# Kernel optimization log

Hardware: AMD Instinct MI355X
Metric: run time of the kernel (lower is better)

Reference implementation:

```python
import jax, jax.numpy as jnp
import numpy as np

N = 50000
F_IN = 128
HID = 16
CLS = 40
NEG_SLOPE = 0.2


def gat_layer(x, src, dst, W, a_src, a_dst, b, heads, out_ch):
    # x: [N, Fin]; src/dst: [E] (self-loops included); W: [Fin, heads*out_ch]
    n = x.shape[0]
    h = (x @ W).reshape(n, heads, out_ch)                    # [N, H, C]
    al_s = jnp.einsum('nhc,hc->nh', h, a_src)                # [N, H]
    al_d = jnp.einsum('nhc,hc->nh', h, a_dst)                # [N, H]
    e = jax.nn.leaky_relu(al_s[src] + al_d[dst], NEG_SLOPE)  # [E, H]
    # segment softmax over incoming edges of each dst node
    m = jax.ops.segment_max(e, dst, num_segments=n)          # [N, H]
    ex = jnp.exp(e - m[dst])
    den = jax.ops.segment_sum(ex, dst, num_segments=n)
    alpha = ex / den[dst]                                    # [E, H]
    out = jax.ops.segment_sum(h[src] * alpha[:, :, None], dst, num_segments=n)
    return out.reshape(n, heads * out_ch) + b


def setup_inputs() -> dict:
    key = jax.random.key(0)
    ks = jax.random.split(key, 16)
    E = 800000
    x = jax.random.normal(ks[0], (N, F_IN), dtype=jnp.float32)
    edge_index = jax.random.randint(ks[1], (2, E), 0, N, dtype=jnp.int64)
    s = 0.1
    W1 = jax.random.normal(ks[2], (F_IN, 7 * HID), dtype=jnp.float32) * s
    a_src1 = jax.random.normal(ks[3], (7, HID), dtype=jnp.float32) * s
    a_dst1 = jax.random.normal(ks[4], (7, HID), dtype=jnp.float32) * s
    b1 = jnp.zeros((7 * HID,), dtype=jnp.float32)
    W2 = jax.random.normal(ks[5], (7 * HID, 6 * HID), dtype=jnp.float32) * s
    a_src2 = jax.random.normal(ks[6], (6, HID), dtype=jnp.float32) * s
    a_dst2 = jax.random.normal(ks[7], (6, HID), dtype=jnp.float32) * s
    b2 = jnp.zeros((6 * HID,), dtype=jnp.float32)
    W3 = jax.random.normal(ks[8], (6 * HID, 6 * CLS), dtype=jnp.float32) * s
    a_src3 = jax.random.normal(ks[9], (6, CLS), dtype=jnp.float32) * s
    a_dst3 = jax.random.normal(ks[10], (6, CLS), dtype=jnp.float32) * s
    b3 = jnp.zeros((6 * CLS,), dtype=jnp.float32)
    return {
        'x': x, 'edge_index': edge_index,
        'W1': W1, 'a_src1': a_src1, 'a_dst1': a_dst1, 'b1': b1,
        'W2': W2, 'a_src2': a_src2, 'a_dst2': a_dst2, 'b2': b2,
        'W3': W3, 'a_src3': a_src3, 'a_dst3': a_dst3, 'b3': b3,
    }


def reference(x, edge_index, W1, a_src1, a_dst1, b1, W2, a_src2, a_dst2, b2, W3, a_src3, a_dst3, b3):
    # add self-loops once (PyG GATConv default add_self_loops=True)
    loops = jnp.arange(N, dtype=edge_index.dtype)
    src = jnp.concatenate([edge_index[0], loops])
    dst = jnp.concatenate([edge_index[1], loops])
    # dropout layers are identity in eval mode
    h = gat_layer(x, src, dst, W1, a_src1, a_dst1, b1, 7, HID)
    h = jax.nn.relu(h)
    h = gat_layer(h, src, dst, W2, a_src2, a_dst2, b2, 6, HID)
    h = jax.nn.relu(h)
    out = gat_layer(h, src, dst, W3, a_src3, a_dst3, b3, 6, CLS)
    return out
```

## Files before the change

kernel.cpp:

```cpp
#include <hip/hip_runtime.h>
#include <hip/hip_fp16.h>
#include <cstdint>

#define NNODES 50000

__device__ inline void wave_lds_fence() {
  asm volatile("s_waitcnt lgkmcnt(0)" ::: "memory");
  __builtin_amdgcn_wave_barrier();
}

__global__ void hist_kernel(const int* __restrict__ ei, int E, int Nn, int* __restrict__ cnt) {
  int i = blockIdx.x * blockDim.x + threadIdx.x;
  int ET = E + Nn;
  if (i >= ET) return;
  int d = (i < E) ? ei[E + i] : (i - E);
  atomicAdd(&cnt[d], 1);
}

__global__ void scan1_kernel(const int* __restrict__ in, int n, int* __restrict__ incl,
                             int* __restrict__ bsum) {
  __shared__ int sd[256];
  int g = blockIdx.x * 256 + threadIdx.x;
  int v = (g < n) ? in[g] : 0;
  sd[threadIdx.x] = v;
  __syncthreads();
  for (int off = 1; off < 256; off <<= 1) {
    int t = (threadIdx.x >= off) ? sd[threadIdx.x - off] : 0;
    __syncthreads();
    sd[threadIdx.x] += t;
    __syncthreads();
  }
  if (g < n) incl[g] = sd[threadIdx.x];
  if (threadIdx.x == 255) bsum[blockIdx.x] = sd[255];
}

__global__ void scan3_kernel(const int* __restrict__ incl, const int* __restrict__ bscan,
                             int n, int* __restrict__ rowptr) {
  int g = blockIdx.x * 256 + threadIdx.x;
  if (g == 0) rowptr[0] = 0;
  if (g < n) {
    int off = (blockIdx.x > 0) ? bscan[blockIdx.x - 1] : 0;
    rowptr[g + 1] = incl[g] + off;
  }
}

__global__ void scatter_kernel(const int* __restrict__ ei, int E, int Nn,
                               const int* __restrict__ rowptr, int* __restrict__ cnt2,
                               int* __restrict__ esorted) {
  int i = blockIdx.x * blockDim.x + threadIdx.x;
  int ET = E + Nn;
  if (i >= ET) return;
  int s, d;
  if (i < E) { s = ei[i]; d = ei[E + i]; }
  else       { s = i - E; d = i - E; }
  int pos = rowptr[d] + atomicAdd(&cnt2[d], 1);
  esorted[pos] = s;
}

template <int FIN, int H, int C, int HCP, int BLOCK>
__global__ __launch_bounds__(BLOCK) void gemm_alpha_kernel(const float* __restrict__ X,
                                                           const float* __restrict__ W,
                                                           const float* __restrict__ a_s,
                                                           const float* __restrict__ a_d,
                                                           __half* __restrict__ Hout,
                                                           float* __restrict__ als8,
                                                           float* __restrict__ ald8) {
  constexpr int HC = H * C;
  constexpr int NT = 16;
  constexpr int TM = 4, TN = 4;
  constexpr int CG = HC / TN;
  constexpr int MAXC = C / TN;
  constexpr int PF = 8;
  static_assert(FIN % (2 * PF) == 0, "FIN must be a multiple of 16");
  __shared__ __align__(16) float xs[FIN * NT];
  __shared__ float redS[NT][H][MAXC];
  __shared__ float redD[NT][H][MAXC];
  const int n0 = blockIdx.x * NT;
  for (int i = threadIdx.x * 4; i < NT * FIN; i += BLOCK * 4) {
    float4 v = *(const float4*)(X + (size_t)n0 * FIN + i);
    int node = i / FIN, k = i % FIN;
    xs[(k + 0) * NT + node] = v.x;
    xs[(k + 1) * NT + node] = v.y;
    xs[(k + 2) * NT + node] = v.z;
    xs[(k + 3) * NT + node] = v.w;
  }
  __syncthreads();
  const int cg = threadIdx.x % CG;
  const int ng = threadIdx.x / CG;
  const bool compute = (ng < NT / TM);
  const int c0 = cg * TN;
  const int i0 = ng * TM;
  if (compute) {
    float acc[TM][TN];
#pragma unroll
    for (int i = 0; i < TM; ++i)
#pragma unroll
      for (int j = 0; j < TN; ++j) acc[i][j] = 0.f;
    const float* Wp = W + c0;
    float4 wb[PF], wn[PF];
#pragma unroll
    for (int j = 0; j < PF; ++j) wb[j] = *(const float4*)(Wp + (size_t)j * HC);
#pragma unroll 1
    for (int k0 = 0; k0 < FIN; k0 += 2 * PF) {
#pragma unroll
      for (int j = 0; j < PF; ++j) wn[j] = *(const float4*)(Wp + (size_t)(k0 + PF + j) * HC);
#pragma unroll
      for (int j = 0; j < PF; ++j) {
        const float4 xv = *(const float4*)(xs + (k0 + j) * NT + i0);
        const float4 wv = wb[j];
        acc[0][0] += xv.x * wv.x; acc[0][1] += xv.x * wv.y; acc[0][2] += xv.x * wv.z; acc[0][3] += xv.x * wv.w;
        acc[1][0] += xv.y * wv.x; acc[1][1] += xv.y * wv.y; acc[1][2] += xv.y * wv.z; acc[1][3] += xv.y * wv.w;
        acc[2][0] += xv.z * wv.x; acc[2][1] += xv.z * wv.y; acc[2][2] += xv.z * wv.z; acc[2][3] += xv.z * wv.w;
        acc[3][0] += xv.w * wv.x; acc[3][1] += xv.w * wv.y; acc[3][2] += xv.w * wv.z; acc[3][3] += xv.w * wv.w;
      }
      const int kp = (k0 + 2 * PF < FIN) ? (k0 + 2 * PF) : 0;
#pragma unroll
      for (int j = 0; j < PF; ++j) wb[j] = *(const float4*)(Wp + (size_t)(kp + j) * HC);
#pragma unroll
      for (int j = 0; j < PF; ++j) {
        const float4 xv = *(const float4*)(xs + (k0 + PF + j) * NT + i0);
        const float4 wv = wn[j];
        acc[0][0] += xv.x * wv.x; acc[0][1] += xv.x * wv.y; acc[0][2] += xv.x * wv.z; acc[0][3] += xv.x * wv.w;
        acc[1][0] += xv.y * wv.x; acc[1][1] += xv.y * wv.y; acc[1][2] += xv.y * wv.z; acc[1][3] += xv.y * wv.w;
        acc[2][0] += xv.z * wv.x; acc[2][1] += xv.z * wv.y; acc[2][2] += xv.z * wv.z; acc[2][3] += xv.z * wv.w;
        acc[3][0] += xv.w * wv.x; acc[3][1] += xv.w * wv.y; acc[3][2] += xv.w * wv.z; acc[3][3] += xv.w * wv.w;
      }
    }
#pragma unroll
    for (int i = 0; i < TM; ++i) {
      union { __half2 h2[2]; uint2 u; } pk;
      pk.h2[0] = __floats2half2_rn(acc[i][0], acc[i][1]);
      pk.h2[1] = __floats2half2_rn(acc[i][2], acc[i][3]);
      *(uint2*)(Hout + (size_t)(n0 + i0 + i) * HCP + c0) = pk.u;
    }
    const int hd = c0 / C;
    const int cidx = (c0 % C) / TN;
    const float4 as4 = *(const float4*)(a_s + c0);
    const float4 ad4 = *(const float4*)(a_d + c0);
#pragma unroll
    for (int i = 0; i < TM; ++i) {
      float ps = acc[i][0] * as4.x + acc[i][1] * as4.y + acc[i][2] * as4.z + acc[i][3] * as4.w;
      float pd = acc[i][0] * ad4.x + acc[i][1] * ad4.y + acc[i][2] * ad4.z + acc[i][3] * ad4.w;
      redS[i0 + i][hd][cidx] = ps;
      redD[i0 + i][hd][cidx] = pd;
    }
  }
  __syncthreads();
  for (int z = threadIdx.x; z < NT * H; z += BLOCK) {
    int n = z / H, h = z % H;
    float ss = 0.f, dd = 0.f;
#pragma unroll
    for (int c = 0; c < MAXC; ++c) { ss += redS[n][h][c]; dd += redD[n][h][c]; }
    als8[(size_t)(n0 + n) * 8 + h] = ss;
    ald8[(size_t)(n0 + n) * 8 + h] = dd;
  }
}

template <int H, int C, int HCP, int RELU>
__global__ __launch_bounds__(256) void agg_kernel(const __half* __restrict__ Hbuf,
                                                  const float* __restrict__ als8,
                                                  const float* __restrict__ ald8,
                                                  const int* __restrict__ rowptr,
                                                  const int* __restrict__ esrc,
                                                  const float* __restrict__ bias,
                                                  float* __restrict__ Out, int n_nodes) {
  constexpr int HC = H * C;
  constexpr int NCHUNK = HC / 8;
  constexpr int GROUPS = (NCHUNK <= 16) ? 4 : 2;
  constexpr int LPG = 64 / GROUPS;
  constexpr int UN = 3;
  constexpr int TPAD = 72;
  const int wave = threadIdx.x >> 6;
  const int lane = threadIdx.x & 63;
  const int grp = lane / LPG;
  const int lg = lane % LPG;
  const int n = blockIdx.x * 4 + wave;
  __shared__ float s_w[4][TPAD * H];
  __shared__ int s_src[4][TPAD];
  if (n >= n_nodes) return;

  if (lane < TPAD - 64) s_src[wave][64 + lane] = 0;
  for (int z = lane; z < (TPAD - 64) * H; z += 64) s_w[wave][64 * H + z] = 0.f;

  const int e0 = rowptr[n];
  const int e1 = rowptr[n + 1];

  float aldn[H];
#pragma unroll
  for (int h = 0; h < H; ++h) aldn[h] = ald8[n * 8 + h];

  const int head = min((lg * 8) / C, H - 1);
  const bool act = lg < NCHUNK;

  float acc[8];
  float lsum = 0.f;
#pragma unroll
  for (int j = 0; j < 8; ++j) acc[j] = 0.f;

  for (int base = e0; base < e1; base += 64) {
    const int cnt = (e1 - base < 64) ? (e1 - base) : 64;
    int sreg = 0;
    if (lane < cnt) sreg = esrc[base + lane];
    s_src[wave][lane] = sreg;
    if (lane < cnt) {
      const float4 qa = *(const float4*)(als8 + (size_t)sreg * 8);
      const float4 qb = *(const float4*)(als8 + (size_t)sreg * 8 + 4);
      const float q[8] = {qa.x, qa.y, qa.z, qa.w, qb.x, qb.y, qb.z, qb.w};
#pragma unroll
      for (int h = 0; h < H; ++h) {
        float v = q[h] + aldn[h];
        v = v > 0.f ? v : 0.2f * v;
        s_w[wave][lane * H + h] = __expf(v);
      }
    } else {
#pragma unroll
      for (int h = 0; h < H; ++h) s_w[wave][lane * H + h] = 0.f;
    }
    wave_lds_fence();
    const int nit = (cnt + GROUPS - 1) / GROUPS;
    for (int i = 0; i < nit; i += UN) {
      int tt[UN], si[UN];
      uint4 v[UN];
      float w[UN];
#pragma unroll
      for (int k = 0; k < UN; ++k) tt[k] = (i + k) * GROUPS + grp;
#pragma unroll
      for (int k = 0; k < UN; ++k) si[k] = s_src[wave][tt[k]];
#pragma unroll
      for (int k = 0; k < UN; ++k)
        if (act) v[k] = *(const uint4*)(Hbuf + (size_t)si[k] * HCP + lg * 8);
#pragma unroll
      for (int k = 0; k < UN; ++k) w[k] = s_w[wave][tt[k] * H + head];
#pragma unroll
      for (int k = 0; k < UN; ++k)
        if (act) {
          const __half2* hp = (const __half2*)&v[k];
          float2 f0 = __half22float2(hp[0]);
          float2 f1 = __half22float2(hp[1]);
          float2 f2 = __half22float2(hp[2]);
          float2 f3 = __half22float2(hp[3]);
          lsum += w[k];
          acc[0] += w[k] * f0.x; acc[1] += w[k] * f0.y;
          acc[2] += w[k] * f1.x; acc[3] += w[k] * f1.y;
          acc[4] += w[k] * f2.x; acc[5] += w[k] * f2.y;
          acc[6] += w[k] * f3.x; acc[7] += w[k] * f3.y;
        }
    }
    wave_lds_fence();
  }

#pragma unroll
  for (int off = LPG; off < 64; off <<= 1) {
    lsum += __shfl_xor(lsum, off);
#pragma unroll
    for (int j = 0; j < 8; ++j) acc[j] += __shfl_xor(acc[j], off);
  }

  if (grp == 0 && act) {
    const float inv = 1.f / lsum;
    const float4 b0 = *(const float4*)(bias + lg * 8);
    const float4 b1 = *(const float4*)(bias + lg * 8 + 4);
    float4 o0, o1;
    o0.x = acc[0] * inv + b0.x; o0.y = acc[1] * inv + b0.y;
    o0.z = acc[2] * inv + b0.z; o0.w = acc[3] * inv + b0.w;
    o1.x = acc[4] * inv + b1.x; o1.y = acc[5] * inv + b1.y;
    o1.z = acc[6] * inv + b1.z; o1.w = acc[7] * inv + b1.w;
    if (RELU) {
      o0.x = fmaxf(o0.x, 0.f); o0.y = fmaxf(o0.y, 0.f);
      o0.z = fmaxf(o0.z, 0.f); o0.w = fmaxf(o0.w, 0.f);
      o1.x = fmaxf(o1.x, 0.f); o1.y = fmaxf(o1.y, 0.f);
      o1.z = fmaxf(o1.z, 0.f); o1.w = fmaxf(o1.w, 0.f);
    }
    *(float4*)(Out + (size_t)n * HC + lg * 8) = o0;
    *(float4*)(Out + (size_t)n * HC + lg * 8 + 4) = o1;
  }
}

extern "C" void kernel_launch(void* const* d_in, const int* in_sizes, int n_in,
                              void* d_out, int out_size, void* d_ws, size_t ws_size,
                              hipStream_t stream) {
  const int N = NNODES;
  const float* x  = (const float*)d_in[0];
  const int* ei   = (const int*)d_in[1];
  const float* W1 = (const float*)d_in[2];
  const float* as1 = (const float*)d_in[3];
  const float* ad1 = (const float*)d_in[4];
  const float* b1  = (const float*)d_in[5];
  const float* W2  = (const float*)d_in[6];
  const float* as2 = (const float*)d_in[7];
  const float* ad2 = (const float*)d_in[8];
  const float* b2  = (const float*)d_in[9];
  const float* W3  = (const float*)d_in[10];
  const float* as3 = (const float*)d_in[11];
  const float* ad3 = (const float*)d_in[12];
  const float* b3  = (const float*)d_in[13];
  float* out = (float*)d_out;
  const int E = in_sizes[1] / 2;
  const int ET = E + N;

  char* ws = (char*)d_ws;
  size_t off = 0;
  auto alloc = [&](size_t bytes) -> char* {
    char* p = ws + off;
    off += (bytes + 255) & ~(size_t)255;
    return p;
  };
  int* cnt     = (int*)alloc((size_t)N * 4);
  int* cnt2    = (int*)alloc((size_t)N * 4);
  int* incl    = (int*)alloc((size_t)N * 4);
  int* bsum    = (int*)alloc(512 * 4);
  int* bscan   = (int*)alloc(256 * 4);
  int* rowptr  = (int*)alloc((size_t)(N + 1) * 4);
  int* esorted = (int*)alloc((size_t)ET * 4);
  float* als   = (float*)alloc((size_t)N * 8 * 4);
  float* ald   = (float*)alloc((size_t)N * 8 * 4);
  __half* hbuf = (__half*)alloc((size_t)N * 256 * 2);
  float* abuf  = (float*)alloc((size_t)N * 112 * 4);

  hipMemsetAsync(cnt, 0, (size_t)N * 4, stream);
  hipMemsetAsync(cnt2, 0, (size_t)N * 4, stream);

  const int B1 = (N + 255) / 256;
  hist_kernel<<<(ET + 255) / 256, 256, 0, stream>>>(ei, E, N, cnt);
  scan1_kernel<<<B1, 256, 0, stream>>>(cnt, N, incl, bsum);
  scan1_kernel<<<1, 256, 0, stream>>>(bsum, B1, bscan, bsum + 256);
  scan3_kernel<<<B1, 256, 0, stream>>>(incl, bscan, N, rowptr);
  scatter_kernel<<<(ET + 255) / 256, 256, 0, stream>>>(ei, E, N, rowptr, cnt2, esorted);

  gemm_alpha_kernel<128, 7, 16, 128, 128><<<N / 16, 128, 0, stream>>>(x, W1, as1, ad1, hbuf, als, ald);
  agg_kernel<7, 16, 128, 1><<<(N + 3) / 4, 256, 0, stream>>>(hbuf, als, ald, rowptr, esorted, b1, abuf, N);
  gemm_alpha_kernel<112, 6, 16, 96, 128><<<N / 16, 128, 0, stream>>>(abuf, W2, as2, ad2, hbuf, als, ald);
  agg_kernel<6, 16, 96, 1><<<(N + 3) / 4, 256, 0, stream>>>(hbuf, als, ald, rowptr, esorted, b2, abuf, N);
  gemm_alpha_kernel<96, 6, 40, 256, 256><<<N / 16, 256, 0, stream>>>(abuf, W3, as3, ad3, hbuf, als, ald);
  agg_kernel<6, 40, 256, 0><<<(N + 3) / 4, 256, 0, stream>>>(hbuf, als, ald, rowptr, esorted, b3, out, N);
}
```

Measured before the change: 459.5 us.

## Stage W tiles through double-buffered LDS in gemm_alpha kernel

Replaces per-thread register prefetch of W rows straight from global memory with cooperative loading of K-tiles of W into a double-buffered shared-memory array. All threads load the next tile into registers while the compute threads work on the current tile, then write it to LDS, with a block barrier after each tile. The goal is to stop each thread re-reading the same W rows from global or L2 memory. The cost is more LDS use, which can lower occupancy, plus a __syncthreads per K-tile.

```diff
diff --git a/kernel.cpp b/kernel.cpp
--- a/kernel.cpp
+++ b/kernel.cpp
@@ -70,12 +70,18 @@
   constexpr int TM = 4, TN = 4;
   constexpr int CG = HC / TN;
   constexpr int MAXC = C / TN;
-  constexpr int PF = 8;
-  static_assert(FIN % (2 * PF) == 0, "FIN must be a multiple of 16");
+  constexpr int KT = 16;
+  constexpr int NTILE = FIN / KT;
+  constexpr int WTILE = KT * HC;
+  constexpr int LPT = (WTILE + BLOCK * 4 - 1) / (BLOCK * 4);
+  static_assert(FIN % KT == 0, "FIN must be a multiple of KT");
+  static_assert(WTILE % 4 == 0, "W tile must be float4-aligned");
   __shared__ __align__(16) float xs[FIN * NT];
+  __shared__ __align__(16) float ws[2][WTILE];
   __shared__ float redS[NT][H][MAXC];
   __shared__ float redD[NT][H][MAXC];
   const int n0 = blockIdx.x * NT;
+
   for (int i = threadIdx.x * 4; i < NT * FIN; i += BLOCK * 4) {
     float4 v = *(const float4*)(X + (size_t)n0 * FIN + i);
     int node = i / FIN, k = i % FIN;
@@ -84,48 +90,61 @@
     xs[(k + 2) * NT + node] = v.z;
     xs[(k + 3) * NT + node] = v.w;
   }
+
+  float4 wr[LPT];
+  auto load_tile = [&](int kt) {
+    const float* src = W + (size_t)kt * WTILE;
+#pragma unroll
+    for (int i = 0; i < LPT; ++i) {
+      int p = (i * BLOCK + threadIdx.x) * 4;
+      if (p < WTILE) wr[i] = *(const float4*)(src + p);
+    }
+  };
+  auto write_tile = [&](int buf) {
+#pragma unroll
+    for (int i = 0; i < LPT; ++i) {
+      int p = (i * BLOCK + threadIdx.x) * 4;
+      if (p < WTILE) *(float4*)(&ws[buf][p]) = wr[i];
+    }
+  };
+
+  load_tile(0);
+  write_tile(0);
   __syncthreads();
+
   const int cg = threadIdx.x % CG;
   const int ng = threadIdx.x / CG;
   const bool compute = (ng < NT / TM);
   const int c0 = cg * TN;
   const int i0 = ng * TM;
-  if (compute) {
-    float acc[TM][TN];
-#pragma unroll
-    for (int i = 0; i < TM; ++i)
-#pragma unroll
-      for (int j = 0; j < TN; ++j) acc[i][j] = 0.f;
-    const float* Wp = W + c0;
-    float4 wb[PF], wn[PF];
-#pragma unroll
-    for (int j = 0; j < PF; ++j) wb[j] = *(const float4*)(Wp + (size_t)j * HC);
+  float acc[TM][TN];
+#pragma unroll
+  for (int i = 0; i < TM; ++i)
+#pragma unroll
+    for (int j = 0; j < TN; ++j) acc[i][j] = 0.f;
+
+  int cur = 0;
 #pragma unroll 1
-    for (int k0 = 0; k0 < FIN; k0 += 2 * PF) {
-#pragma unroll
-      for (int j = 0; j < PF; ++j) wn[j] = *(const float4*)(Wp + (size_t)(k0 + PF + j) * HC);
-#pragma unroll
-      for (int j = 0; j < PF; ++j) {
-        const float4 xv = *(const float4*)(xs + (k0 + j) * NT + i0);
-        const float4 wv = wb[j];
+  for (int kt = 0; kt < NTILE; ++kt) {
+    if (kt + 1 < NTILE) load_tile(kt + 1);
+    if (compute) {
+      const float* wp = &ws[cur][0] + c0;
+#pragma unroll
+      for (int k = 0; k < KT; ++k) {
+        const float4 wv = *(const float4*)(wp + k * HC);
+        const float4 xv = *(const float4*)(xs + (kt * KT + k) * NT + i0);
         acc[0][0] += xv.x * wv.x; acc[0][1] += xv.x * wv.y; acc[0][2] += xv.x * wv.z; acc[0][3] += xv.x * wv.w;
         acc[1][0] += xv.y * wv.x; acc[1][1] += xv.y * wv.y; acc[1][2] += xv.y * wv.z; acc[1][3] += xv.y * wv.w;
         acc[2][0] += xv.z * wv.x; acc[2][1] += xv.z * wv.y; acc[2][2] += xv.z * wv.z; acc[2][3] += xv.z * wv.w;
         acc[3][0] += xv.w * wv.x; acc[3][1] += xv.w * wv.y; acc[3][2] += xv.w * wv.z; acc[3][3] += xv.w * wv.w;
       }
-      const int kp = (k0 + 2 * PF < FIN) ? (k0 + 2 * PF) : 0;
-#pragma unroll
-      for (int j = 0; j < PF; ++j) wb[j] = *(const float4*)(Wp + (size_t)(kp + j) * HC);
-#pragma unroll
-      for (int j = 0; j < PF; ++j) {
-        const float4 xv = *(const float4*)(xs + (k0 + PF + j) * NT + i0);
-        const float4 wv = wn[j];
-        acc[0][0] += xv.x * wv.x; acc[0][1] += xv.x * wv.y; acc[0][2] += xv.x * wv.z; acc[0][3] += xv.x * wv.w;
-        acc[1][0] += xv.y * wv.x; acc[1][1] += xv.y * wv.y; acc[1][2] += xv.y * wv.z; acc[1][3] += xv.y * wv.w;
-        acc[2][0] += xv.z * wv.x; acc[2][1] += xv.z * wv.y; acc[2][2] += xv.z * wv.z; acc[2][3] += xv.z * wv.w;
-        acc[3][0] += xv.w * wv.x; acc[3][1] += xv.w * wv.y; acc[3][2] += xv.w * wv.z; acc[3][3] += xv.w * wv.w;
-      }
-    }
+    }
+    if (kt + 1 < NTILE) write_tile(cur ^ 1);
+    __syncthreads();
+    cur ^= 1;
+  }
+
+  if (compute) {
 #pragma unroll
     for (int i = 0; i < TM; ++i) {
       union { __half2 h2[2]; uint2 u; } pk;
```

New measurement: 566.5 us. 23.3% more time.
